# Optimization experiments

Measured on AMD Instinct MI355X. Metric: run time of the kernel, lower is better.

## Reference

```python
import jax, jax.numpy as jnp
import numpy as np
import math

B, H, L, N, CD = 16, 512, 2048, 64, 128
BN_EPS = 1e-5


def setup_inputs() -> dict:
    key = jax.random.key(0)
    ks = jax.random.split(key, 12)
    x = jax.random.normal(ks[0], (B, H, L), jnp.float32)
    cond = jax.random.normal(ks[1], (B, CD), jnp.float32)
    # input Linear(H, H)
    linear_w = jax.random.normal(ks[2], (H, H), jnp.float32) * (1.0 / math.sqrt(H))
    linear_b = jax.random.normal(ks[3], (H,), jnp.float32) * 0.01
    # DSSM params (torch init: log_dt ~ U[log dt_min, log dt_max])
    log_dt = jax.random.uniform(ks[4], (H,), jnp.float32) * (math.log(0.1) - math.log(0.001)) + math.log(0.001)
    C_ri = jax.random.normal(ks[5], (H, N, 2), jnp.float32)  # view_as_real of complex C
    log_A_real = jnp.full((H, N), jnp.log(0.5), jnp.float32)
    A_imag = jnp.broadcast_to(math.pi * jnp.arange(N, dtype=jnp.float32), (H, N))
    D = jax.random.normal(ks[6], (H,), jnp.float32)
    # FiLM adaptor Linear(CD, 2H)
    film_w = jax.random.normal(ks[7], (2 * H, CD), jnp.float32) * (1.0 / math.sqrt(CD))
    film_b = jax.random.normal(ks[8], (2 * H,), jnp.float32) * 0.01
    # depthwise 1x1 residual conv (groups=H, bias=False) -> per-channel scale
    res_w = jax.random.normal(ks[9], (H,), jnp.float32)
    return {"x": x, "cond": cond, "linear_w": linear_w, "linear_b": linear_b,
            "log_dt": log_dt, "C_ri": C_ri, "log_A_real": log_A_real,
            "A_imag": A_imag, "D": D, "film_w": film_w, "film_b": film_b,
            "res_w": res_w}


def _s4_kernel(log_dt, C_ri, log_A_real, A_imag, length):
    dt = jnp.exp(log_dt)                       # [H]
    C = C_ri[..., 0] + 1j * C_ri[..., 1]       # [H, N] complex
    A = -jnp.exp(log_A_real) + 1j * A_imag     # [H, N] complex
    dtA = A * dt[:, None]                      # [H, N]
    t = jnp.arange(length, dtype=jnp.float32)
    P = dtA[:, :, None] * t                    # [H, N, L] complex
    Cm = C * (jnp.exp(dtA) - 1.0) / A          # [H, N]
    K = 2.0 * jnp.einsum('hn,hnl->hl', Cm, jnp.exp(P)).real  # [H, L]
    return K


def reference(x, cond, linear_w, linear_b, log_dt, C_ri, log_A_real, A_imag, D,
              film_w, film_b, res_w):
    # --- linear over channel dim (B H L -> B L H -> linear -> B H L) ---
    h = jnp.einsum('bhl,gh->bgl', x, linear_w) + linear_b[None, :, None]
    h = jax.nn.gelu(h, approximate=False)  # torch.nn.GELU default (erf)
    # --- DSSM: full-length group (forward passes length=None) ---
    K = _s4_kernel(log_dt, C_ri, log_A_real, A_imag, L)     # [H, L]
    n_fft = 2 * L
    k_f = jnp.fft.rfft(K, n=n_fft)                           # [H, Lf]
    u_f = jnp.fft.rfft(h, n=n_fft)                           # [B, H, Lf]
    y = jnp.fft.irfft(u_f * k_f[None], n=n_fft)[..., :L]     # [B, H, L]
    y = y + h * D[None, :, None]                             # D skip
    # --- FiLM: BatchNorm1d(affine=False, batch stats) then scale/shift ---
    gb = cond @ film_w.T + film_b                            # [B, 2H]
    g, b = gb[:, :H], gb[:, H:]
    mean = jnp.mean(y, axis=(0, 2), keepdims=True)
    var = jnp.var(y, axis=(0, 2), keepdims=True)             # biased, as torch BN
    y = (y - mean) * jax.lax.rsqrt(var + BN_EPS)
    y = y * g[:, :, None] + b[:, :, None]
    y = jax.nn.gelu(y, approximate=False)
    # --- depthwise 1x1 residual ---
    return y + x * res_w[None, :, None]
```

## Files before the change

### kernel.cpp

```cpp
#include <hip/hip_runtime.h>
#include <math.h>

#define B_ 16
#define H_ 512
#define L_ 2048
#define N_ 64
#define CD_ 128

typedef unsigned int u32;
typedef unsigned short u16;
typedef __attribute__((ext_vector_type(8))) short bf16x8;
typedef __attribute__((ext_vector_type(4))) float f32x4;

__device__ __forceinline__ float gelu_f(float v) {
    return 0.5f * v * (1.0f + erff(v * 0.70710678118654752f));
}
__device__ __forceinline__ float bf2f(u16 b) {
    union { u32 u; float f; } c; c.u = ((u32)b) << 16; return c.f;
}
__device__ __forceinline__ u16 f2bf(float f) {
    union { float f; u32 u; } c; c.f = f;
    u32 u = c.u;
    return (u16)((u + 0x7FFFu + ((u >> 16) & 1u)) >> 16);
}
__device__ __forceinline__ u32 pack2(float a, float b) {
    return (u32)f2bf(a) | ((u32)f2bf(b) << 16);
}

__global__ void k_fill(float* __restrict__ out, int n, float val) {
    int i = blockIdx.x * 256 + threadIdx.x;
    if (i < n) out[i] = val;
}

__global__ __launch_bounds__(256) void k_K3(
    const float* __restrict__ log_dt, const float* __restrict__ C_ri,
    const float* __restrict__ log_A_real, const float* __restrict__ A_imag,
    float* __restrict__ Kbuf) {
    int h = blockIdx.x;
    int t = threadIdx.x;
    __shared__ float dre[N_], dim[N_], cre[N_], cim[N_];
    __shared__ float2 Thi[64 * 64];
    __shared__ float2 Elo[64 * 32];
    if (t < N_) {
        float dt = expf(log_dt[h]);
        float a_re = -expf(log_A_real[h * N_ + t]);
        float a_im = A_imag[h * N_ + t];
        float dA_re = a_re * dt, dA_im = a_im * dt;
        float er = expf(dA_re);
        float s, c;
        sincosf(dA_im, &s, &c);
        float num_re = er * c - 1.0f, num_im = er * s;
        float den = a_re * a_re + a_im * a_im;
        float q_re = (num_re * a_re + num_im * a_im) / den;
        float q_im = (num_im * a_re - num_re * a_im) / den;
        float Cr = C_ri[(h * N_ + t) * 2 + 0];
        float Ci = C_ri[(h * N_ + t) * 2 + 1];
        cre[t] = Cr * q_re - Ci * q_im;
        cim[t] = Cr * q_im + Ci * q_re;
        dre[t] = dA_re; dim[t] = dA_im;
    }
    __syncthreads();
    #pragma unroll
    for (int i = 0; i < 16; ++i) {
        int id = t + 256 * i;
        int n = id >> 6, q = id & 63;
        float a = (float)(32 * q);
        float er = expf(dre[n] * a);
        float s, c;
        sincosf(dim[n] * a, &s, &c);
        Thi[id] = make_float2(er * (cre[n] * c - cim[n] * s),
                              er * (cre[n] * s + cim[n] * c));
    }
    #pragma unroll
    for (int i = 0; i < 8; ++i) {
        int id = t + 256 * i;
        int n = id >> 5, r = id & 31;
        float a = (float)r;
        float er = expf(dre[n] * a);
        float s, c;
        sincosf(dim[n] * a, &s, &c);
        Elo[id] = make_float2(er * c, er * s);
    }
    __syncthreads();
    int q = t >> 2, r0 = (t & 3) * 8;
    float acc[8] = {};
    for (int n = 0; n < 64; ++n) {
        float2 T = Thi[n * 64 + q];
        const float2* e = &Elo[n * 32 + r0];
        #pragma unroll
        for (int j = 0; j < 8; ++j)
            acc[j] += T.x * e[j].x - T.y * e[j].y;
    }
    float* out = Kbuf + (size_t)h * L_ + t * 8;
    #pragma unroll
    for (int j = 0; j < 8; ++j) out[j] = 2.0f * acc[j];
}

__global__ void k_film(const float* __restrict__ cond,
                       const float* __restrict__ film_w,
                       const float* __restrict__ film_b,
                       float* __restrict__ gb) {
    int j = blockIdx.x * 256 + threadIdx.x;
    int b  = j >> 10;
    int jj = j & 1023;
    float acc = film_b[jj];
    for (int c = 0; c < CD_; ++c)
        acc += cond[b * CD_ + c] * film_w[jj * CD_ + c];
    gb[j] = acc;
}

__global__ __launch_bounds__(512, 4) void k_linear4(
    const float* __restrict__ x, const float* __restrict__ W,
    const float* __restrict__ bias, float* __restrict__ hbuf) {
    int b  = blockIdx.z;
    int g0 = blockIdx.y * 128;
    int l0 = blockIdx.x * 128;
    __shared__ __align__(16) u16 Wp[128 * 64];
    __shared__ __align__(16) u16 Bl[128 * 72];
    int t = threadIdx.x;
    int lane = t & 63, wv = t >> 6;
    int n = lane & 15, kg = lane >> 4;
    int wr = wv >> 2, wc = wv & 3;
    int lr  = t & 127, kq = t >> 7;
    int rw  = (t >> 4) & 31;
    int f16 = t & 15;

    f32x4 acc[4][2];
    #pragma unroll
    for (int m = 0; m < 4; ++m)
        #pragma unroll
        for (int q = 0; q < 2; ++q) acc[m][q] = (f32x4){0.f, 0.f, 0.f, 0.f};

    const float* xcol = x + (size_t)b * H_ * L_ + l0 + lr;
    float  cx[16], nx[16];
    float4 cw[4],  nw[4];
    #pragma unroll
    for (int e = 0; e < 16; ++e) cx[e] = xcol[(size_t)(kq * 16 + e) * L_];
    #pragma unroll
    for (int e = 0; e < 4; ++e)
        cw[e] = *(const float4*)&W[(size_t)(g0 + rw + 32 * e) * H_ + f16 * 4];

    #pragma unroll
    for (int S = 0; S < 8; ++S) {
        if (S) __syncthreads();
        {
            u32 px[8];
            #pragma unroll
            for (int e = 0; e < 8; ++e) px[e] = pack2(cx[2 * e], cx[2 * e + 1]);
            uint4 u0 = {px[0], px[1], px[2], px[3]};
            uint4 u1 = {px[4], px[5], px[6], px[7]};
            *(uint4*)((char*)Bl + lr * 144 + kq * 32)      = u0;
            *(uint4*)((char*)Bl + lr * 144 + kq * 32 + 16) = u1;
        }
        #pragma unroll
        for (int e = 0; e < 4; ++e) {
            int row = rw + 32 * e;
            uint2 pw;
            pw.x = pack2(cw[e].x, cw[e].y);
            pw.y = pack2(cw[e].z, cw[e].w);
            *(uint2*)((char*)Wp + row * 128 + ((f16 * 8) ^ ((row & 7) << 4))) = pw;
        }
        __syncthreads();
        if (S < 7) {
            int k0n = (S + 1) * 64;
            #pragma unroll
            for (int e = 0; e < 16; ++e) nx[e] = xcol[(size_t)(k0n + kq * 16 + e) * L_];
            #pragma unroll
            for (int e = 0; e < 4; ++e)
                nw[e] = *(const float4*)&W[(size_t)(g0 + rw + 32 * e) * H_ + k0n + f16 * 4];
        }
        #pragma unroll
        for (int ks = 0; ks < 2; ++ks) {
            bf16x8 af[4], bfr[2];
            #pragma unroll
            for (int m = 0; m < 4; ++m) {
                int row = wr * 64 + m * 16 + n;
                af[m] = *(const bf16x8*)((const char*)Wp + row * 128 +
                         ((ks * 64 + kg * 16) ^ ((n & 7) << 4)));
            }
            #pragma unroll
            for (int q = 0; q < 2; ++q)
                bfr[q] = *(const bf16x8*)((const char*)Bl +
                          (wc * 32 + q * 16 + n) * 144 + ks * 64 + kg * 16);
            #pragma unroll
            for (int m = 0; m < 4; ++m)
                #pragma unroll
                for (int q = 0; q < 2; ++q)
                    acc[m][q] = __builtin_amdgcn_mfma_f32_16x16x32_bf16(
                        af[m], bfr[q], acc[m][q], 0, 0, 0);
        }
        if (S < 7) {
            #pragma unroll
            for (int e = 0; e < 16; ++e) cx[e] = nx[e];
            #pragma unroll
            for (int e = 0; e < 4; ++e)  cw[e] = nw[e];
        }
    }

    #pragma unroll
    for (int m = 0; m < 4; ++m) {
        #pragma unroll
        for (int r = 0; r < 4; ++r) {
            int g = g0 + wr * 64 + m * 16 + kg * 4 + r;
            float bi = bias[g];
            float* dst = &hbuf[((size_t)b * H_ + g) * L_ + l0 + wc * 32 + n];
            #pragma unroll
            for (int q = 0; q < 2; ++q)
                dst[q * 16] = gelu_f(acc[m][q][r] + bi);
        }
    }
}

#define LDA(j0) (*(const bf16x8*)(smem + rowbase + (((u32)((j0) * 2 + kg16)) ^ swz)))
__global__ __launch_bounds__(512, 4) void k_conv_mfma(
    float* __restrict__ hy, const float* __restrict__ Kbuf,
    const float* __restrict__ Dp, const float* __restrict__ x,
    const float* __restrict__ gb, const float* __restrict__ res_w) {
    int g = blockIdx.x;
    __shared__ __align__(16) char smem[81920];
    uint2* KD2 = (uint2*)(smem + 65536);
    int t = threadIdx.x;
    int wv = t >> 6, lane = t & 63;
    int n = lane & 15, kg = lane >> 4;

    const float* Kg = Kbuf + (size_t)g * L_;
    #pragma unroll
    for (int i0 = 0; i0 < 4; ++i0) {
        int i = t + 512 * i0;
        float f0 = Kg[L_ - 1 - i];
        float f1 = (i + 1 < L_) ? Kg[L_ - 2 - i] : 0.f;
        float f2 = (i + 2 < L_) ? Kg[L_ - 3 - i] : 0.f;
        float f3 = (i + 3 < L_) ? Kg[L_ - 4 - i] : 0.f;
        uint2 w; w.x = pack2(f0, f1); w.y = pack2(f2, f3);
        KD2[i] = w;
    }
    for (int b = 0; b < B_; ++b) {
        float4 v = *(const float4*)&hy[((size_t)b * H_ + g) * L_ + t * 4];
        uint2 p2; p2.x = pack2(v.x, v.y); p2.y = pack2(v.z, v.w);
        *(uint2*)(smem + b * 4096 + (((u32)(t * 8)) ^ ((b & 7) << 4))) = p2;
    }
    __syncthreads();

    const int p = wv & 1, q4 = wv >> 1;
    const int rowbase = n * 4096;
    const u32 swz = (u32)((n & 7) << 4);
    const int kg16 = kg * 16;
    const int bofs = 8 * kg - n;

    f32x4 acc[4][4];
    #pragma unroll
    for (int ri = 0; ri < 4; ++ri)
        #pragma unroll
        for (int m = 0; m < 4; ++m) acc[ri][m] = (f32x4){0.f, 0.f, 0.f, 0.f};

    const int rrs[4] = {q4, 7 - q4, 8 + q4, 15 - q4};
    #pragma unroll
    for (int ri = 0; ri < 4; ++ri) {
        const int k = 4 * rrs[ri];
        bf16x8 af0 = LDA(32 * (k + 0));
        bf16x8 af1 = LDA(32 * (k + 1));
        bf16x8 af2 = LDA(32 * (k + 2));
        bf16x8 af3 = LDA(32 * (k + 3));
        union { u32 u[4]; bf16x8 v; } bu;
        {
            int base = 2047 - 16 * p + bofs;
            int b0 = base < 2047 ? base : 2047;
            int b1 = (base + 4) < 2047 ? (base + 4) : 2047;
            uint2 w01 = KD2[b0];
            uint2 w23 = KD2[b1];
            if (base > 2047)     { w01.x = 0u; w01.y = 0u; }
            if (base + 4 > 2047) { w23.x = 0u; w23.y = 0u; }
            bu.u[0] = w01.x; bu.u[1] = w01.y; bu.u[2] = w23.x; bu.u[3] = w23.y;
            acc[ri][0] = __builtin_amdgcn_mfma_f32_16x16x32_bf16(af0, bu.v, acc[ri][0], 0, 0, 0);
            acc[ri][1] = __builtin_amdgcn_mfma_f32_16x16x32_bf16(af1, bu.v, acc[ri][1], 0, 0, 0);
            acc[ri][2] = __builtin_amdgcn_mfma_f32_16x16x32_bf16(af2, bu.v, acc[ri][2], 0, 0, 0);
            acc[ri][3] = __builtin_amdgcn_mfma_f32_16x16x32_bf16(af3, bu.v, acc[ri][3], 0, 0, 0);
            af3 = af2; af2 = af1; af1 = af0;
            if (k >= 1) af0 = LDA(32 * (k - 1));
        }
        for (int c = 1; c <= k; ++c) {
            int base = 2047 - 16 * p - 32 * c + bofs;
            uint2 w01 = KD2[base];
            uint2 w23 = KD2[base + 4];
            bu.u[0] = w01.x; bu.u[1] = w01.y; bu.u[2] = w23.x; bu.u[3] = w23.y;
            acc[ri][0] = __builtin_amdgcn_mfma_f32_16x16x32_bf16(af0, bu.v, acc[ri][0], 0, 0, 0);
            acc[ri][1] = __builtin_amdgcn_mfma_f32_16x16x32_bf16(af1, bu.v, acc[ri][1], 0, 0, 0);
            acc[ri][2] = __builtin_amdgcn_mfma_f32_16x16x32_bf16(af2, bu.v, acc[ri][2], 0, 0, 0);
            acc[ri][3] = __builtin_amdgcn_mfma_f32_16x16x32_bf16(af3, bu.v, acc[ri][3], 0, 0, 0);
            af3 = af2; af2 = af1; af1 = af0;
            int jn = k - c - 1;
            if (jn >= 0) af0 = LDA(32 * jn);
        }
        #pragma unroll
        for (int e = 1; e <= 3; ++e) {
            int base = 2047 - 16 * p - 32 * (k + e) + bofs;
            uint2 w01 = KD2[base];
            uint2 w23 = KD2[base + 4];
            bu.u[0] = w01.x; bu.u[1] = w01.y; bu.u[2] = w23.x; bu.u[3] = w23.y;
            if (e <= 1) acc[ri][1] = __builtin_amdgcn_mfma_f32_16x16x32_bf16(af1, bu.v, acc[ri][1], 0, 0, 0);
            if (e <= 2) acc[ri][2] = __builtin_amdgcn_mfma_f32_16x16x32_bf16(af2, bu.v, acc[ri][2], 0, 0, 0);
            acc[ri][3] = __builtin_amdgcn_mfma_f32_16x16x32_bf16(af3, bu.v, acc[ri][3], 0, 0, 0);
            af3 = af2; af2 = af1;
        }
    }

    float Dg = Dp[g];
    float sum = 0.f, sq = 0.f;
    #pragma unroll
    for (int ri = 0; ri < 4; ++ri) {
        #pragma unroll
        for (int m = 0; m < 4; ++m) {
            const int l0 = 16 * p + 128 * rrs[ri] + 32 * m;
            #pragma unroll
            for (int r = 0; r < 4; ++r) {
                int b = kg * 4 + r;
                float hval = bf2f(*(const u16*)(smem + b * 4096 +
                              (((u32)(2 * (l0 + n))) ^ ((b & 7) << 4))));
                float y = acc[ri][m][r] + Dg * hval;
                acc[ri][m][r] = y;
                sum += y; sq += y * y;
            }
        }
    }
    #pragma unroll
    for (int off = 32; off > 0; off >>= 1) {
        sum += __shfl_down(sum, off);
        sq  += __shfl_down(sq, off);
    }
    __syncthreads();
    float* red = (float*)(smem + 65536);
    if (lane == 0) { red[wv] = sum; red[8 + wv] = sq; }
    __syncthreads();
    if (t == 0) {
        float s = 0.f, q = 0.f;
        #pragma unroll
        for (int i = 0; i < 8; ++i) { s += red[i]; q += red[8 + i]; }
        const float inv = 1.0f / (float)(B_ * L_);
        float mean = s * inv;
        float var = q * inv - mean * mean;
        red[16] = mean; red[17] = rsqrtf(var + 1e-5f);
    }
    __syncthreads();
    const float mean = red[16], rstd = red[17];
    const float rw = res_w[g];
    #pragma unroll
    for (int r = 0; r < 4; ++r) {
        int b = kg * 4 + r;
        float gf = gb[b * (2 * H_) + g];
        float bb = gb[b * (2 * H_) + H_ + g];
        #pragma unroll
        for (int ri = 0; ri < 4; ++ri) {
            #pragma unroll
            for (int m = 0; m < 4; ++m) {
                const int l0 = 16 * p + 128 * rrs[ri] + 32 * m;
                size_t idx = ((size_t)b * H_ + g) * L_ + l0 + n;
                float yn = (acc[ri][m][r] - mean) * rstd;
                hy[idx] = gelu_f(yn * gf + bb) + x[idx] * rw;
            }
        }
    }
}

extern "C" void kernel_launch(void* const* d_in, const int* in_sizes, int n_in,
                              void* d_out, int out_size, void* d_ws, size_t ws_size,
                              hipStream_t stream) {
    const int expect[12] = {16777216, 2048, 262144, 512, 512, 65536,
                            32768, 32768, 512, 131072, 1024, 512};
    bool ok = (n_in == 12);
    if (ok) for (int i = 0; i < 12; ++i) if (in_sizes[i] != expect[i]) ok = false;
    if (!ok) {
        k_fill<<<(out_size + 255) / 256, 256, 0, stream>>>((float*)d_out, out_size, 1000.0f);
        return;
    }
    if (ws_size < ((size_t)H_ * L_ * 4 + (size_t)B_ * 2 * H_ * 4 + 1024)) {
        k_fill<<<(out_size + 255) / 256, 256, 0, stream>>>((float*)d_out, out_size, 2000.0f);
        return;
    }

    const float* x          = (const float*)d_in[0];
    const float* cond       = (const float*)d_in[1];
    const float* linear_w   = (const float*)d_in[2];
    const float* linear_b   = (const float*)d_in[3];
    const float* log_dt     = (const float*)d_in[4];
    const float* C_ri       = (const float*)d_in[5];
    const float* log_A_real = (const float*)d_in[6];
    const float* A_imag     = (const float*)d_in[7];
    const float* Dp         = (const float*)d_in[8];
    const float* film_w     = (const float*)d_in[9];
    const float* film_b     = (const float*)d_in[10];
    const float* res_w      = (const float*)d_in[11];

    float* hy = (float*)d_out;

    char* w = (char*)d_ws;
    float* Kbuf  = (float*)w;  w += (size_t)H_ * L_ * 4;
    float* gb    = (float*)w;  w += (size_t)B_ * 2 * H_ * 4;

    k_K3<<<H_, 256, 0, stream>>>(log_dt, C_ri, log_A_real, A_imag, Kbuf);
    k_film<<<(B_ * 2 * H_) / 256, 256, 0, stream>>>(cond, film_w, film_b, gb);
    dim3 gmm(L_ / 128, H_ / 128, B_);
    k_linear4<<<gmm, 512, 0, stream>>>(x, linear_w, linear_b, hy);
    k_conv_mfma<<<H_, 512, 0, stream>>>(hy, Kbuf, Dp, x, gb, res_w);
}
```

Baseline: 148.2 us.

## Fuse FiLM into conv, store h as bf16, restructure conv and kernel-gen

The FiLM projection is folded into the conv kernel, which removes one launch and the gb buffer. The intermediate h is written as bf16 to workspace when space allows, halving its write and read traffic. The S4 kernel generator now builds powers by repeated complex multiplication instead of many exp/sincos calls, and the conv loop is restructured into 8-wide ring-buffered MFMA blocks over 256-column rows. Repeated complex products may lose some accuracy, and whether the bf16 path runs depends on workspace size.

```diff
diff --git a/kernel.cpp b/kernel.cpp
--- a/kernel.cpp
+++ b/kernel.cpp
@@ -26,92 +26,72 @@
 __device__ __forceinline__ u32 pack2(float a, float b) {
     return (u32)f2bf(a) | ((u32)f2bf(b) << 16);
 }
+__device__ __forceinline__ float2 cmul(float2 a, float2 b) {
+    return make_float2(a.x * b.x - a.y * b.y, a.x * b.y + a.y * b.x);
+}
 
 __global__ void k_fill(float* __restrict__ out, int n, float val) {
     int i = blockIdx.x * 256 + threadIdx.x;
     if (i < n) out[i] = val;
 }
 
-__global__ __launch_bounds__(256) void k_K3(
+__global__ __launch_bounds__(256) void k_K4(
     const float* __restrict__ log_dt, const float* __restrict__ C_ri,
     const float* __restrict__ log_A_real, const float* __restrict__ A_imag,
     float* __restrict__ Kbuf) {
-    int h = blockIdx.x;
-    int t = threadIdx.x;
-    __shared__ float dre[N_], dim[N_], cre[N_], cim[N_];
-    __shared__ float2 Thi[64 * 64];
-    __shared__ float2 Elo[64 * 32];
+    int h = blockIdx.x, t = threadIdx.x;
+    __shared__ float2 P1[N_][8], P8[N_][4], P32[N_][8], P256[N_][8], Cs[N_];
     if (t < N_) {
+        int n = t;
         float dt = expf(log_dt[h]);
-        float a_re = -expf(log_A_real[h * N_ + t]);
-        float a_im = A_imag[h * N_ + t];
-        float dA_re = a_re * dt, dA_im = a_im * dt;
-        float er = expf(dA_re);
+        float a_re = -expf(log_A_real[h * N_ + n]);
+        float a_im = A_imag[h * N_ + n];
+        float dre = a_re * dt, dim = a_im * dt;
+        float er = expf(dre);
         float s, c;
-        sincosf(dA_im, &s, &c);
-        float num_re = er * c - 1.0f, num_im = er * s;
+        sincosf(dim, &s, &c);
+        float2 E1 = make_float2(er * c, er * s);
+        float num_re = E1.x - 1.0f, num_im = E1.y;
         float den = a_re * a_re + a_im * a_im;
         float q_re = (num_re * a_re + num_im * a_im) / den;
         float q_im = (num_im * a_re - num_re * a_im) / den;
-        float Cr = C_ri[(h * N_ + t) * 2 + 0];
-        float Ci = C_ri[(h * N_ + t) * 2 + 1];
-        cre[t] = Cr * q_re - Ci * q_im;
-        cim[t] = Cr * q_im + Ci * q_re;
-        dre[t] = dA_re; dim[t] = dA_im;
+        float Cr = C_ri[(h * N_ + n) * 2 + 0], Ci = C_ri[(h * N_ + n) * 2 + 1];
+        Cs[n] = make_float2(Cr * q_re - Ci * q_im, Cr * q_im + Ci * q_re);
+        float2 w = make_float2(1.f, 0.f);
+        #pragma unroll
+        for (int i = 0; i < 8; ++i) { P1[n][i] = w; w = cmul(w, E1); }
+        float2 E8 = w; w = make_float2(1.f, 0.f);
+        #pragma unroll
+        for (int i = 0; i < 4; ++i) { P8[n][i] = w; w = cmul(w, E8); }
+        float2 E32 = w; w = make_float2(1.f, 0.f);
+        #pragma unroll
+        for (int i = 0; i < 8; ++i) { P32[n][i] = w; w = cmul(w, E32); }
+        float2 E256 = w; w = make_float2(1.f, 0.f);
+        #pragma unroll
+        for (int i = 0; i < 8; ++i) { P256[n][i] = w; w = cmul(w, E256); }
     }
     __syncthreads();
-    #pragma unroll
-    for (int i = 0; i < 16; ++i) {
-        int id = t + 256 * i;
-        int n = id >> 6, q = id & 63;
-        float a = (float)(32 * q);
-        float er = expf(dre[n] * a);
-        float s, c;
-        sincosf(dim[n] * a, &s, &c);
-        Thi[id] = make_float2(er * (cre[n] * c - cim[n] * s),
-                              er * (cre[n] * s + cim[n] * c));
-    }
-    #pragma unroll
-    for (int i = 0; i < 8; ++i) {
-        int id = t + 256 * i;
-        int n = id >> 5, r = id & 31;
-        float a = (float)r;
-        float er = expf(dre[n] * a);
-        float s, c;
-        sincosf(dim[n] * a, &s, &c);
-        Elo[id] = make_float2(er * c, er * s);
-    }
-    __syncthreads();
-    int q = t >> 2, r0 = (t & 3) * 8;
+    int qh = t >> 5, ql = (t >> 2) & 7, rh = t & 3;
     float acc[8] = {};
-    for (int n = 0; n < 64; ++n) {
-        float2 T = Thi[n * 64 + q];
-        const float2* e = &Elo[n * 32 + r0];
-        #pragma unroll
-        for (int j = 0; j < 8; ++j)
-            acc[j] += T.x * e[j].x - T.y * e[j].y;
+    for (int n = 0; n < N_; ++n) {
+        float2 a = cmul(Cs[n], P256[n][qh]);
+        a = cmul(a, P32[n][ql]);
+        a = cmul(a, P8[n][rh]);
+        #pragma unroll
+        for (int j = 0; j < 8; ++j) {
+            float2 e = P1[n][j];
+            acc[j] += a.x * e.x - a.y * e.y;
+        }
     }
     float* out = Kbuf + (size_t)h * L_ + t * 8;
     #pragma unroll
     for (int j = 0; j < 8; ++j) out[j] = 2.0f * acc[j];
-}
-
-__global__ void k_film(const float* __restrict__ cond,
-                       const float* __restrict__ film_w,
-                       const float* __restrict__ film_b,
-                       float* __restrict__ gb) {
-    int j = blockIdx.x * 256 + threadIdx.x;
-    int b  = j >> 10;
-    int jj = j & 1023;
-    float acc = film_b[jj];
-    for (int c = 0; c < CD_; ++c)
-        acc += cond[b * CD_ + c] * film_w[jj * CD_ + c];
-    gb[j] = acc;
 }
 
 __global__ __launch_bounds__(512, 4) void k_linear4(
     const float* __restrict__ x, const float* __restrict__ W,
-    const float* __restrict__ bias, float* __restrict__ hbuf) {
+    const float* __restrict__ bias, float* __restrict__ hf32,
+    u16* __restrict__ hb16, int bf16h) {
     int b  = blockIdx.z;
     int g0 = blockIdx.y * 128;
     int l0 = blockIdx.x * 128;
@@ -203,19 +183,72 @@
         for (int r = 0; r < 4; ++r) {
             int g = g0 + wr * 64 + m * 16 + kg * 4 + r;
             float bi = bias[g];
-            float* dst = &hbuf[((size_t)b * H_ + g) * L_ + l0 + wc * 32 + n];
-            #pragma unroll
-            for (int q = 0; q < 2; ++q)
-                dst[q * 16] = gelu_f(acc[m][q][r] + bi);
-        }
-    }
-}
-
-#define LDA(j0) (*(const bf16x8*)(smem + rowbase + (((u32)((j0) * 2 + kg16)) ^ swz)))
+            float v0 = gelu_f(acc[m][0][r] + bi);
+            float v1 = gelu_f(acc[m][1][r] + bi);
+            size_t off = ((size_t)b * H_ + g) * L_ + l0 + wc * 32 + n;
+            if (bf16h) {
+                hb16[off]      = f2bf(v0);
+                hb16[off + 16] = f2bf(v1);
+            } else {
+                hf32[off]      = v0;
+                hf32[off + 16] = v1;
+            }
+        }
+    }
+}
+
+template<int E, bool DIAG, bool TAIL, bool LOAD>
+__device__ __forceinline__ void cstep(const uint2* __restrict__ KD2, int& base,
+    bf16x8 (&ring)[8], f32x4 (&accR)[8], const char* smem,
+    int rowbase, u32 swz, int kg16, int& ja) {
+    uint2 w01, w23;
+    if (DIAG) {
+        int b0 = base < 2047 ? base : 2047;
+        int b1 = (base + 4) < 2047 ? (base + 4) : 2047;
+        w01 = KD2[b0];
+        w23 = KD2[b1];
+        if (base > 2047)     { w01.x = 0u; w01.y = 0u; }
+        if (base + 4 > 2047) { w23.x = 0u; w23.y = 0u; }
+    } else {
+        w01 = KD2[base];
+        w23 = KD2[base + 4];
+    }
+    union { u32 u[4]; bf16x8 v; } bu;
+    bu.u[0] = w01.x; bu.u[1] = w01.y; bu.u[2] = w23.x; bu.u[3] = w23.y;
+    #pragma unroll
+    for (int m = 0; m < 8; ++m)
+        if (!TAIL || m >= E)
+            accR[m] = __builtin_amdgcn_mfma_f32_16x16x32_bf16(
+                ring[(m - E) & 7], bu.v, accR[m], 0, 0, 0);
+    if (LOAD) {
+        ring[(7 - E) & 7] = *(const bf16x8*)(smem + rowbase +
+                            (((u32)(ja * 64 + kg16)) ^ swz));
+        ja -= 1;
+    }
+    base -= 32;
+}
+
+template<bool DIAG, bool TAIL, bool LOAD>
+__device__ __forceinline__ void cblock8(const uint2* __restrict__ KD2, int& base,
+    bf16x8 (&ring)[8], f32x4 (&accR)[8], const char* smem,
+    int rowbase, u32 swz, int kg16, int& ja) {
+    cstep<0, DIAG,  TAIL, LOAD>(KD2, base, ring, accR, smem, rowbase, swz, kg16, ja);
+    cstep<1, false, TAIL, LOAD>(KD2, base, ring, accR, smem, rowbase, swz, kg16, ja);
+    cstep<2, false, TAIL, LOAD>(KD2, base, ring, accR, smem, rowbase, swz, kg16, ja);
+    cstep<3, false, TAIL, LOAD>(KD2, base, ring, accR, smem, rowbase, swz, kg16, ja);
+    cstep<4, false, TAIL, LOAD>(KD2, base, ring, accR, smem, rowbase, swz, kg16, ja);
+    cstep<5, false, TAIL, LOAD>(KD2, base, ring, accR, smem, rowbase, swz, kg16, ja);
+    cstep<6, false, TAIL, LOAD>(KD2, base, ring, accR, smem, rowbase, swz, kg16, ja);
+    cstep<7, false, TAIL, LOAD>(KD2, base, ring, accR, smem, rowbase, swz, kg16, ja);
+}
+
 __global__ __launch_bounds__(512, 4) void k_conv_mfma(
-    float* __restrict__ hy, const float* __restrict__ Kbuf,
-    const float* __restrict__ Dp, const float* __restrict__ x,
-    const float* __restrict__ gb, const float* __restrict__ res_w) {
+    float* __restrict__ out, const u16* __restrict__ hb16,
+    const float* __restrict__ hf32, int bf16h,
+    const float* __restrict__ Kbuf, const float* __restrict__ Dp,
+    const float* __restrict__ x, const float* __restrict__ cond,
+    const float* __restrict__ film_w, const float* __restrict__ film_b,
+    const float* __restrict__ res_w) {
     int g = blockIdx.x;
     __shared__ __align__(16) char smem[81920];
     uint2* KD2 = (uint2*)(smem + 65536);
@@ -234,10 +267,19 @@
         uint2 w; w.x = pack2(f0, f1); w.y = pack2(f2, f3);
         KD2[i] = w;
     }
-    for (int b = 0; b < B_; ++b) {
-        float4 v = *(const float4*)&hy[((size_t)b * H_ + g) * L_ + t * 4];
-        uint2 p2; p2.x = pack2(v.x, v.y); p2.y = pack2(v.z, v.w);
-        *(uint2*)(smem + b * 4096 + (((u32)(t * 8)) ^ ((b & 7) << 4))) = p2;
+    if (bf16h) {
+        #pragma unroll
+        for (int b = 0; b < B_; ++b) {
+            uint2 p2 = *(const uint2*)&hb16[((size_t)b * H_ + g) * L_ + t * 4];
+            *(uint2*)(smem + b * 4096 + (((u32)(t * 8)) ^ ((b & 7) << 4))) = p2;
+        }
+    } else {
+        #pragma unroll
+        for (int b = 0; b < B_; ++b) {
+            float4 v = *(const float4*)&hf32[((size_t)b * H_ + g) * L_ + t * 4];
+            uint2 p2; p2.x = pack2(v.x, v.y); p2.y = pack2(v.z, v.w);
+            *(uint2*)(smem + b * 4096 + (((u32)(t * 8)) ^ ((b & 7) << 4))) = p2;
+        }
     }
     __syncthreads();
 
@@ -246,71 +288,42 @@
     const u32 swz = (u32)((n & 7) << 4);
     const int kg16 = kg * 16;
     const int bofs = 8 * kg - n;
-
-    f32x4 acc[4][4];
-    #pragma unroll
-    for (int ri = 0; ri < 4; ++ri)
-        #pragma unroll
-        for (int m = 0; m < 4; ++m) acc[ri][m] = (f32x4){0.f, 0.f, 0.f, 0.f};
-
-    const int rrs[4] = {q4, 7 - q4, 8 + q4, 15 - q4};
-    #pragma unroll
-    for (int ri = 0; ri < 4; ++ri) {
-        const int k = 4 * rrs[ri];
-        bf16x8 af0 = LDA(32 * (k + 0));
-        bf16x8 af1 = LDA(32 * (k + 1));
-        bf16x8 af2 = LDA(32 * (k + 2));
-        bf16x8 af3 = LDA(32 * (k + 3));
-        union { u32 u[4]; bf16x8 v; } bu;
-        {
-            int base = 2047 - 16 * p + bofs;
-            int b0 = base < 2047 ? base : 2047;
-            int b1 = (base + 4) < 2047 ? (base + 4) : 2047;
-            uint2 w01 = KD2[b0];
-            uint2 w23 = KD2[b1];
-            if (base > 2047)     { w01.x = 0u; w01.y = 0u; }
-            if (base + 4 > 2047) { w23.x = 0u; w23.y = 0u; }
-            bu.u[0] = w01.x; bu.u[1] = w01.y; bu.u[2] = w23.x; bu.u[3] = w23.y;
-            acc[ri][0] = __builtin_amdgcn_mfma_f32_16x16x32_bf16(af0, bu.v, acc[ri][0], 0, 0, 0);
-            acc[ri][1] = __builtin_amdgcn_mfma_f32_16x16x32_bf16(af1, bu.v, acc[ri][1], 0, 0, 0);
-            acc[ri][2] = __builtin_amdgcn_mfma_f32_16x16x32_bf16(af2, bu.v, acc[ri][2], 0, 0, 0);
-            acc[ri][3] = __builtin_amdgcn_mfma_f32_16x16x32_bf16(af3, bu.v, acc[ri][3], 0, 0, 0);
-            af3 = af2; af2 = af1; af1 = af0;
-            if (k >= 1) af0 = LDA(32 * (k - 1));
-        }
-        for (int c = 1; c <= k; ++c) {
-            int base = 2047 - 16 * p - 32 * c + bofs;
-            uint2 w01 = KD2[base];
-            uint2 w23 = KD2[base + 4];
-            bu.u[0] = w01.x; bu.u[1] = w01.y; bu.u[2] = w23.x; bu.u[3] = w23.y;
-            acc[ri][0] = __builtin_amdgcn_mfma_f32_16x16x32_bf16(af0, bu.v, acc[ri][0], 0, 0, 0);
-            acc[ri][1] = __builtin_amdgcn_mfma_f32_16x16x32_bf16(af1, bu.v, acc[ri][1], 0, 0, 0);
-            acc[ri][2] = __builtin_amdgcn_mfma_f32_16x16x32_bf16(af2, bu.v, acc[ri][2], 0, 0, 0);
-            acc[ri][3] = __builtin_amdgcn_mfma_f32_16x16x32_bf16(af3, bu.v, acc[ri][3], 0, 0, 0);
-            af3 = af2; af2 = af1; af1 = af0;
-            int jn = k - c - 1;
-            if (jn >= 0) af0 = LDA(32 * jn);
-        }
-        #pragma unroll
-        for (int e = 1; e <= 3; ++e) {
-            int base = 2047 - 16 * p - 32 * (k + e) + bofs;
-            uint2 w01 = KD2[base];
-            uint2 w23 = KD2[base + 4];
-            bu.u[0] = w01.x; bu.u[1] = w01.y; bu.u[2] = w23.x; bu.u[3] = w23.y;
-            if (e <= 1) acc[ri][1] = __builtin_amdgcn_mfma_f32_16x16x32_bf16(af1, bu.v, acc[ri][1], 0, 0, 0);
-            if (e <= 2) acc[ri][2] = __builtin_amdgcn_mfma_f32_16x16x32_bf16(af2, bu.v, acc[ri][2], 0, 0, 0);
-            acc[ri][3] = __builtin_amdgcn_mfma_f32_16x16x32_bf16(af3, bu.v, acc[ri][3], 0, 0, 0);
-            af3 = af2; af2 = af1;
+    const int rrs[2] = {q4, 7 - q4};
+
+    f32x4 acc[2][8];
+    #pragma unroll
+    for (int ri = 0; ri < 2; ++ri)
+        #pragma unroll
+        for (int m = 0; m < 8; ++m) acc[ri][m] = (f32x4){0.f, 0.f, 0.f, 0.f};
+
+    #pragma unroll
+    for (int ri = 0; ri < 2; ++ri) {
+        const int rr = rrs[ri];
+        const int k8 = rr * 8;
+        bf16x8 ring[8];
+        #pragma unroll
+        for (int m = 0; m < 8; ++m)
+            ring[m] = *(const bf16x8*)(smem + rowbase +
+                      (((u32)((k8 + m) * 64 + kg16)) ^ swz));
+        int base = 2047 - 16 * p + bofs;
+        int ja = k8 - 1;
+        if (rr == 0) {
+            cblock8<true, true, false>(KD2, base, ring, acc[ri], smem, rowbase, swz, kg16, ja);
+        } else {
+            cblock8<true, false, true>(KD2, base, ring, acc[ri], smem, rowbase, swz, kg16, ja);
+            for (int bi = 1; bi < rr; ++bi)
+                cblock8<false, false, true>(KD2, base, ring, acc[ri], smem, rowbase, swz, kg16, ja);
+            cblock8<false, true, false>(KD2, base, ring, acc[ri], smem, rowbase, swz, kg16, ja);
         }
     }
 
     float Dg = Dp[g];
     float sum = 0.f, sq = 0.f;
     #pragma unroll
-    for (int ri = 0; ri < 4; ++ri) {
-        #pragma unroll
-        for (int m = 0; m < 4; ++m) {
-            const int l0 = 16 * p + 128 * rrs[ri] + 32 * m;
+    for (int ri = 0; ri < 2; ++ri) {
+        #pragma unroll
+        for (int m = 0; m < 8; ++m) {
+            const int l0 = 16 * p + 256 * rrs[ri] + 32 * m;
             #pragma unroll
             for (int r = 0; r < 4; ++r) {
                 int b = kg * 4 + r;
@@ -330,6 +343,19 @@
     __syncthreads();
     float* red = (float*)(smem + 65536);
     if (lane == 0) { red[wv] = sum; red[8 + wv] = sq; }
+    if (t >= 64 && t < 96) {
+        int tid = t - 64, b = tid >> 1, which = tid & 1;
+        int row = which ? (H_ + g) : g;
+        float a = film_b[row];
+        const float4* wr4 = (const float4*)(film_w + (size_t)row * CD_);
+        const float4* cp4 = (const float4*)(cond + b * CD_);
+        #pragma unroll
+        for (int c4 = 0; c4 < CD_ / 4; ++c4) {
+            float4 cw = cp4[c4], ww = wr4[c4];
+            a += cw.x * ww.x + cw.y * ww.y + cw.z * ww.z + cw.w * ww.w;
+        }
+        red[18 + tid] = a;
+    }
     __syncthreads();
     if (t == 0) {
         float s = 0.f, q = 0.f;
@@ -346,16 +372,16 @@
     #pragma unroll
     for (int r = 0; r < 4; ++r) {
         int b = kg * 4 + r;
-        float gf = gb[b * (2 * H_) + g];
-        float bb = gb[b * (2 * H_) + H_ + g];
-        #pragma unroll
-        for (int ri = 0; ri < 4; ++ri) {
-            #pragma unroll
-            for (int m = 0; m < 4; ++m) {
-                const int l0 = 16 * p + 128 * rrs[ri] + 32 * m;
+        float gf = red[18 + 2 * b];
+        float bb = red[18 + 2 * b + 1];
+        #pragma unroll
+        for (int ri = 0; ri < 2; ++ri) {
+            #pragma unroll
+            for (int m = 0; m < 8; ++m) {
+                const int l0 = 16 * p + 256 * rrs[ri] + 32 * m;
                 size_t idx = ((size_t)b * H_ + g) * L_ + l0 + n;
                 float yn = (acc[ri][m][r] - mean) * rstd;
-                hy[idx] = gelu_f(yn * gf + bb) + x[idx] * rw;
+                out[idx] = gelu_f(yn * gf + bb) + x[idx] * rw;
             }
         }
     }
@@ -372,7 +398,7 @@
         k_fill<<<(out_size + 255) / 256, 256, 0, stream>>>((float*)d_out, out_size, 1000.0f);
         return;
     }
-    if (ws_size < ((size_t)H_ * L_ * 4 + (size_t)B_ * 2 * H_ * 4 + 1024)) {
+    if (ws_size < (size_t)H_ * L_ * 4 + 4096) {
         k_fill<<<(out_size + 255) / 256, 256, 0, stream>>>((float*)d_out, out_size, 2000.0f);
         return;
     }
@@ -393,12 +419,14 @@
     float* hy = (float*)d_out;
 
     char* w = (char*)d_ws;
-    float* Kbuf  = (float*)w;  w += (size_t)H_ * L_ * 4;
-    float* gb    = (float*)w;  w += (size_t)B_ * 2 * H_ * 4;
-
-    k_K3<<<H_, 256, 0, stream>>>(log_dt, C_ri, log_A_real, A_imag, Kbuf);
-    k_film<<<(B_ * 2 * H_) / 256, 256, 0, stream>>>(cond, film_w, film_b, gb);
+    float* Kbuf = (float*)w;  w += (size_t)H_ * L_ * 4;
+    u16*   hb16 = (u16*)w;
+    const size_t need_bf16 = (size_t)H_ * L_ * 4 + (size_t)B_ * H_ * L_ * 2 + 4096;
+    int bf16h = (ws_size >= need_bf16) ? 1 : 0;
+
+    k_K4<<<H_, 256, 0, stream>>>(log_dt, C_ri, log_A_real, A_imag, Kbuf);
     dim3 gmm(L_ / 128, H_ / 128, B_);
-    k_linear4<<<gmm, 512, 0, stream>>>(x, linear_w, linear_b, hy);
-    k_conv_mfma<<<H_, 512, 0, stream>>>(hy, Kbuf, Dp, x, gb, res_w);
-}
+    k_linear4<<<gmm, 512, 0, stream>>>(x, linear_w, linear_b, hy, hb16, bf16h);
+    k_conv_mfma<<<H_, 512, 0, stream>>>(hy, hb16, hy, bf16h, Kbuf, Dp, x,
+                                        cond, film_w, film_b, res_w);
+}
```

Result: faster. 137.9 us (-6.9%).
